# Kernel tuning notes

Hardware: AMD Instinct MI355X
Metric: run time of the kernel (lower is better)

The kernel has to match this reference:

```python
import jax, jax.numpy as jnp
import numpy as np

B, C_IN, C_OUT = 8, 64, 64
H, W = 256, 256
FH, FW = 16, 16  # patch grid from weight map spatial dims
HYPER_PARAMS = C_OUT * C_IN  # kernel_size=1, groups=1


def setup_inputs() -> dict:
    key = jax.random.key(0)
    kx, ks = jax.random.split(key)
    x = jax.random.normal(kx, (B, C_IN, H, W), dtype=jnp.float32)
    # s is the hypernetwork-generated per-patch weight map [b, out*in, fh, fw]
    s = jax.random.normal(ks, (B, HYPER_PARAMS, FH, FW), dtype=jnp.float32)
    return {"x": x, "s": s}


def reference(x, s):
    b, c, h, w = x.shape
    fh, fw = s.shape[-2], s.shape[-1]
    ph, pw = h // fh, w // fw
    out_ch = s.shape[1] // c  # hyper_params = out_ch * c (1x1 kernel, groups=1)
    # weight.permute(0,2,3,1).reshape(b*fh*fw*out, in, 1, 1) -> per-patch [out, in]
    Wp = jnp.transpose(s, (0, 2, 3, 1)).reshape(b, fh, fw, out_ch, c)
    # x.view(b,c,fh,ph,fw,pw).permute(0,2,4,1,3,5) -> per-patch blocks [b,fh,fw,c,ph,pw]
    xp = jnp.transpose(x.reshape(b, c, fh, ph, fw, pw), (0, 2, 4, 1, 3, 5))
    # grouped 1x1 conv over b*fh*fw groups == batched small matmul per patch
    y = jnp.einsum('bijoc,bijcpq->bijopq', Wp, xp)
    # .view(b,fh,fw,-1,ph,pw).permute(0,3,1,4,2,5).reshape(b,-1,h,w)
    return jnp.transpose(y, (0, 3, 1, 4, 2, 5)).reshape(b, out_ch, h, w)
```

## Files before the change

kernel.cpp:

```cpp
#include <hip/hip_runtime.h>

#define NB 8

typedef __bf16 bf16x8 __attribute__((ext_vector_type(8)));
typedef float  f32x4  __attribute__((ext_vector_type(4)));

__global__ __launch_bounds__(256) void fused_kernel(
    const float* __restrict__ x,
    const float* __restrict__ s,
    float* __restrict__ out)
{
    __shared__ char smem[49152];

    const int bid = blockIdx.x;
    const int b   = bid & 7;
    const int pjp = (bid >> 3) & 7;
    const int pi  = bid >> 6;
    const int t   = threadIdx.x;
    const int lane = t & 63;
    const int wv   = t >> 6;
    const int q    = lane & 15;
    const int hi   = lane >> 4;
    const int pat  = wv & 1;
    const int pgrp = wv >> 1;
    const int w0   = pjp * 32;
    const int pj0  = pjp * 2;

    const int sp_p = t >> 6;
    const int swq  = (t >> 3) & 7;
    const int sco  = t & 7;
    const float* xbase = x + (size_t)b * 4194304 + (size_t)(sco * 8) * 65536
                           + w0 + swq * 4;

    {
        const float2* sp2 = (const float2*)(s + (size_t)b * 1048576 + pi * 16 + pj0);
        #pragma unroll
        for (int k = 0; k < 16; ++k) {
            const int r = t + k * 256;
            float2 v = sp2[(size_t)r * 128];
            const int o = r >> 6, c = r & 63;
            const int ent = ((o >> 4) * 2 + (c >> 5)) * 64 + ((c >> 3) & 3) * 16 + (o & 15);
            const int byt = ent * 16 + (c & 7) * 2;
            *(__bf16*)(smem + byt)        = (__bf16)v.x;
            *(__bf16*)(smem + 8192 + byt) = (__bf16)v.y;
        }
    }

    {
        const int row0 = pi * 16;
        f32x4 v[8];
        #pragma unroll
        for (int cc = 0; cc < 8; ++cc)
            v[cc] = *(const f32x4*)(xbase + (size_t)cc * 65536
                                    + (size_t)(row0 + sp_p) * 256);
        #pragma unroll
        for (int i = 0; i < 4; ++i) {
            const int w = swq * 4 + i;
            bf16x8 e;
            #pragma unroll
            for (int cc = 0; cc < 8; ++cc) e[cc] = (__bf16)v[cc][i];
            *(bf16x8*)(smem + 16384 + sp_p * 4096 + w * 128
                       + ((sco * 16) ^ ((w & 7) << 4) ^ (sp_p << 4))) = e;
        }
    }
    __syncthreads();

    bf16x8 a[4][2];
    #pragma unroll
    for (int mt = 0; mt < 4; ++mt)
        #pragma unroll
        for (int kk = 0; kk < 2; ++kk)
            a[mt][kk] = *(const bf16x8*)(smem + pat * 8192
                          + ((mt * 2 + kk) * 64 + lane) * 16);

    int cur = 0;
    #pragma unroll
    for (int tile = 0; tile < 4; ++tile) {
        const int row0 = pi * 16 + tile * 4;
        char* bufc = smem + 16384 + cur * 16384;

        f32x4 nv[8];
        if (tile < 3) {
            #pragma unroll
            for (int cc = 0; cc < 8; ++cc)
                nv[cc] = *(const f32x4*)(xbase + (size_t)cc * 65536
                                         + (size_t)(row0 + 4 + sp_p) * 256);
        }
        __builtin_amdgcn_sched_barrier(0);

        bf16x8 bf[2][2];
        #pragma unroll
        for (int pp = 0; pp < 2; ++pp) {
            const int p = pgrp * 2 + pp;
            const int w = pat * 16 + q;
            #pragma unroll
            for (int kk = 0; kk < 2; ++kk) {
                const int co = kk * 4 + hi;
                bf[pp][kk] = *(const bf16x8*)(bufc + p * 4096 + w * 128
                              + ((co * 16) ^ ((w & 7) << 4) ^ (p << 4)));
            }
        }

        f32x4 acc[2][4];
        #pragma unroll
        for (int pp = 0; pp < 2; ++pp)
            #pragma unroll
            for (int mt = 0; mt < 4; ++mt) {
                acc[pp][mt] = (f32x4){0.f, 0.f, 0.f, 0.f};
                acc[pp][mt] = __builtin_amdgcn_mfma_f32_16x16x32_bf16(
                    a[mt][0], bf[pp][0], acc[pp][mt], 0, 0, 0);
                acc[pp][mt] = __builtin_amdgcn_mfma_f32_16x16x32_bf16(
                    a[mt][1], bf[pp][1], acc[pp][mt], 0, 0, 0);
            }

        if (tile < 3) {
            char* bufn = smem + 16384 + (cur ^ 1) * 16384;
            #pragma unroll
            for (int i = 0; i < 4; ++i) {
                const int w = swq * 4 + i;
                bf16x8 e;
                #pragma unroll
                for (int cc = 0; cc < 8; ++cc) e[cc] = (__bf16)nv[cc][i];
                *(bf16x8*)(bufn + sp_p * 4096 + w * 128
                           + ((sco * 16) ^ ((w & 7) << 4) ^ (sp_p << 4))) = e;
            }
        }
        __syncthreads();

        float* ef = (float*)bufc;
        #pragma unroll
        for (int h2 = 0; h2 < 2; ++h2) {
            #pragma unroll
            for (int pp = 0; pp < 2; ++pp) {
                const int p = pgrp * 2 + pp;
                const int w = pat * 16 + q;
                #pragma unroll
                for (int m2 = 0; m2 < 2; ++m2) {
                    const int mt = h2 * 2 + m2;
                    #pragma unroll
                    for (int r = 0; r < 4; ++r) {
                        const int o2 = m2 * 16 + hi * 4 + r;
                        ef[(o2 * 4 + p) * 32 + (w ^ ((o2 & 7) << 2))] = acc[pp][mt][r];
                    }
                }
            }
            __syncthreads();
            #pragma unroll
            for (int ps = 0; ps < 4; ++ps) {
                const int line = ps * 32 + (t >> 3);
                const int o2 = line >> 2, p = line & 3;
                f32x4 vv = *(const f32x4*)&ef[(o2 * 4 + p) * 32
                                              + ((sco * 4) ^ ((o2 & 7) << 2))];
                *(f32x4*)(out + (size_t)(b * 64 + h2 * 32 + o2) * 65536
                              + (size_t)(row0 + p) * 256 + w0 + sco * 4) = vv;
            }
            __syncthreads();
        }
        cur ^= 1;
    }
}

extern "C" void kernel_launch(void* const* d_in, const int* in_sizes, int n_in,
                              void* d_out, int out_size, void* d_ws, size_t ws_size,
                              hipStream_t stream)
{
    (void)in_sizes; (void)n_in; (void)out_size; (void)d_ws; (void)ws_size;
    const float* x = (const float*)d_in[0];
    const float* s = (const float*)d_in[1];
    float* out = (float*)d_out;

    fused_kernel<<<dim3(1024), dim3(256), 0, stream>>>(x, s, out);
}
```

Baseline: 77.59 us.

## Split each patch pair across two blocks and load all x rows upfront

Each block now handles 8 rows of a patch pair instead of 16, which doubles the grid to 2048 blocks. All global loads for x and s are issued at the start, before any conversion. The double-buffered 4-tile pipeline is replaced by a single tile with more MFMA work per wave. The goal is more memory parallelism and occupancy (launch bounds of 2) to hide latency, at the cost of loading the s weights twice per patch and holding more registers.

```diff
diff --git a/kernel.cpp b/kernel.cpp
--- a/kernel.cpp
+++ b/kernel.cpp
@@ -5,62 +5,70 @@
 typedef __bf16 bf16x8 __attribute__((ext_vector_type(8)));
 typedef float  f32x4  __attribute__((ext_vector_type(4)));
 
-__global__ __launch_bounds__(256) void fused_kernel(
+__global__ __launch_bounds__(256, 2) void fused_gemm(
     const float* __restrict__ x,
     const float* __restrict__ s,
     float* __restrict__ out)
 {
     __shared__ char smem[49152];
+    char* smemX = smem + 16384;
+    float* ef   = (float*)(smem + 16384);
 
     const int bid = blockIdx.x;
     const int b   = bid & 7;
-    const int pjp = (bid >> 3) & 7;
-    const int pi  = bid >> 6;
+    const int pi  = (bid >> 3) & 15;
+    const int ph  = (bid >> 7) & 1;
+    const int pjp = (bid >> 8) & 7;
     const int t   = threadIdx.x;
     const int lane = t & 63;
     const int wv   = t >> 6;
+    const int pat  = wv & 1;
+    const int wrow = wv >> 1;
     const int q    = lane & 15;
     const int hi   = lane >> 4;
-    const int pat  = wv & 1;
-    const int pgrp = wv >> 1;
     const int w0   = pjp * 32;
-    const int pj0  = pjp * 2;
+    const int row0 = pi * 16 + ph * 8;
 
-    const int sp_p = t >> 6;
-    const int swq  = (t >> 3) & 7;
-    const int sco  = t & 7;
-    const float* xbase = x + (size_t)b * 4194304 + (size_t)(sco * 8) * 65536
-                           + w0 + swq * 4;
+    const int swq = lane & 7;
+    const int sco = lane >> 3;
+    const float* xrowbase = x + (size_t)(b * 64 + sco * 8) * 65536
+                              + (size_t)row0 * 256 + w0 + swq * 4;
+    f32x4 xv[16];
+    #pragma unroll
+    for (int pp = 0; pp < 2; ++pp)
+        #pragma unroll
+        for (int cc = 0; cc < 8; ++cc)
+            xv[pp * 8 + cc] = *(const f32x4*)(xrowbase + (size_t)cc * 65536
+                                              + (size_t)(wv * 2 + pp) * 256);
 
-    {
-        const float2* sp2 = (const float2*)(s + (size_t)b * 1048576 + pi * 16 + pj0);
-        #pragma unroll
-        for (int k = 0; k < 16; ++k) {
-            const int r = t + k * 256;
-            float2 v = sp2[(size_t)r * 128];
-            const int o = r >> 6, c = r & 63;
-            const int ent = ((o >> 4) * 2 + (c >> 5)) * 64 + ((c >> 3) & 3) * 16 + (o & 15);
-            const int byt = ent * 16 + (c & 7) * 2;
-            *(__bf16*)(smem + byt)        = (__bf16)v.x;
-            *(__bf16*)(smem + 8192 + byt) = (__bf16)v.y;
-        }
+    const float2* sp2 = (const float2*)(s + (size_t)b * 1048576 + pi * 16 + pjp * 2);
+    float2 sv[16];
+    #pragma unroll
+    for (int k = 0; k < 16; ++k)
+        sv[k] = sp2[(size_t)(t + k * 256) * 128];
+
+    #pragma unroll
+    for (int k = 0; k < 16; ++k) {
+        const int r = t + k * 256;
+        const int o = r >> 6, c = r & 63;
+        const int ent = ((o >> 4) * 2 + (c >> 5)) * 64 + ((c >> 3) & 3) * 16 + (o & 15);
+        const int byt = ent * 16 + (c & 7) * 2;
+        *(__bf16*)(smem + byt)        = (__bf16)sv[k].x;
+        *(__bf16*)(smem + 8192 + byt) = (__bf16)sv[k].y;
     }
 
-    {
-        const int row0 = pi * 16;
-        f32x4 v[8];
-        #pragma unroll
-        for (int cc = 0; cc < 8; ++cc)
-            v[cc] = *(const f32x4*)(xbase + (size_t)cc * 65536
-                                    + (size_t)(row0 + sp_p) * 256);
+    #pragma unroll
+    for (int pp = 0; pp < 2; ++pp) {
+        const int p = wv * 2 + pp;
         #pragma unroll
         for (int i = 0; i < 4; ++i) {
             const int w = swq * 4 + i;
             bf16x8 e;
             #pragma unroll
-            for (int cc = 0; cc < 8; ++cc) e[cc] = (__bf16)v[cc][i];
-            *(bf16x8*)(smem + 16384 + sp_p * 4096 + w * 128
-                       + ((sco * 16) ^ ((w & 7) << 4) ^ (sp_p << 4))) = e;
+            for (int cc = 0; cc < 8; ++cc)
+                e[cc] = (__bf16)xv[pp * 8 + cc][i];
+            *(bf16x8*)(smemX + p * 4096 + w * 128
+                       + ((sco * 16) ^ ((w & 7) << 4) ^ ((p & 7) << 4))) = e;
         }
     }
     __syncthreads();
@@ -73,90 +81,68 @@
             a[mt][kk] = *(const bf16x8*)(smem + pat * 8192
                           + ((mt * 2 + kk) * 64 + lane) * 16);
 
-    int cur = 0;
+    bf16x8 bfrag[4][2];
     #pragma unroll
-    for (int tile = 0; tile < 4; ++tile) {
-        const int row0 = pi * 16 + tile * 4;
-        char* bufc = smem + 16384 + cur * 16384;
+    for (int nt = 0; nt < 4; ++nt) {
+        const int p = wrow * 4 + nt;
+        const int w = pat * 16 + q;
+        #pragma unroll
+        for (int kk = 0; kk < 2; ++kk) {
+            const int co = kk * 4 + hi;
+            bfrag[nt][kk] = *(const bf16x8*)(smemX + p * 4096 + w * 128
+                            + ((co * 16) ^ ((w & 7) << 4) ^ ((p & 7) << 4)));
+        }
+    }
+    __syncthreads();
 
-        f32x4 nv[8];
-        if (tile < 3) {
+    const int u2t = t >> 3;
+    const int wq2 = t & 7;
+    #pragma unroll
+    for (int h2 = 0; h2 < 2; ++h2) {
+        f32x4 acc[2][4];
+        #pragma unroll
+        for (int m2 = 0; m2 < 2; ++m2)
             #pragma unroll
-            for (int cc = 0; cc < 8; ++cc)
-                nv[cc] = *(const f32x4*)(xbase + (size_t)cc * 65536
-                                         + (size_t)(row0 + 4 + sp_p) * 256);
-        }
-        __builtin_amdgcn_sched_barrier(0);
+            for (int nt = 0; nt < 4; ++nt)
+                acc[m2][nt] = (f32x4){0.f, 0.f, 0.f, 0.f};
 
-        bf16x8 bf[2][2];
         #pragma unroll
-        for (int pp = 0; pp < 2; ++pp) {
-            const int p = pgrp * 2 + pp;
-            const int w = pat * 16 + q;
+        for (int m2 = 0; m2 < 2; ++m2) {
+            const int mt = h2 * 2 + m2;
             #pragma unroll
-            for (int kk = 0; kk < 2; ++kk) {
-                const int co = kk * 4 + hi;
-                bf[pp][kk] = *(const bf16x8*)(bufc + p * 4096 + w * 128
-                              + ((co * 16) ^ ((w & 7) << 4) ^ (p << 4)));
+            for (int nt = 0; nt < 4; ++nt) {
+                acc[m2][nt] = __builtin_amdgcn_mfma_f32_16x16x32_bf16(
+                    a[mt][0], bfrag[nt][0], acc[m2][nt], 0, 0, 0);
+                acc[m2][nt] = __builtin_amdgcn_mfma_f32_16x16x32_bf16(
+                    a[mt][1], bfrag[nt][1], acc[m2][nt], 0, 0, 0);
             }
         }
 
-        f32x4 acc[2][4];
         #pragma unroll
-        for (int pp = 0; pp < 2; ++pp)
+        for (int m2 = 0; m2 < 2; ++m2)
             #pragma unroll
-            for (int mt = 0; mt < 4; ++mt) {
-                acc[pp][mt] = (f32x4){0.f, 0.f, 0.f, 0.f};
-                acc[pp][mt] = __builtin_amdgcn_mfma_f32_16x16x32_bf16(
-                    a[mt][0], bf[pp][0], acc[pp][mt], 0, 0, 0);
-                acc[pp][mt] = __builtin_amdgcn_mfma_f32_16x16x32_bf16(
-                    a[mt][1], bf[pp][1], acc[pp][mt], 0, 0, 0);
+            for (int nt = 0; nt < 4; ++nt) {
+                const int p = wrow * 4 + nt;
+                #pragma unroll
+                for (int r = 0; r < 4; ++r) {
+                    const int o2 = m2 * 16 + hi * 4 + r;
+                    const int w  = pat * 16 + q;
+                    ef[(o2 * 8 + p) * 32 + (w ^ ((o2 & 7) << 2))] = acc[m2][nt][r];
+                }
             }
-
-        if (tile < 3) {
-            char* bufn = smem + 16384 + (cur ^ 1) * 16384;
-            #pragma unroll
-            for (int i = 0; i < 4; ++i) {
-                const int w = swq * 4 + i;
-                bf16x8 e;
-                #pragma unroll
-                for (int cc = 0; cc < 8; ++cc) e[cc] = (__bf16)nv[cc][i];
-                *(bf16x8*)(bufn + sp_p * 4096 + w * 128
-                           + ((sco * 16) ^ ((w & 7) << 4) ^ (sp_p << 4))) = e;
-            }
-        }
         __syncthreads();
 
-        float* ef = (float*)bufc;
         #pragma unroll
-        for (int h2 = 0; h2 < 2; ++h2) {
-            #pragma unroll
-            for (int pp = 0; pp < 2; ++pp) {
-                const int p = pgrp * 2 + pp;
-                const int w = pat * 16 + q;
-                #pragma unroll
-                for (int m2 = 0; m2 < 2; ++m2) {
-                    const int mt = h2 * 2 + m2;
-                    #pragma unroll
-                    for (int r = 0; r < 4; ++r) {
-                        const int o2 = m2 * 16 + hi * 4 + r;
-                        ef[(o2 * 4 + p) * 32 + (w ^ ((o2 & 7) << 2))] = acc[pp][mt][r];
-                    }
-                }
-            }
-            __syncthreads();
-            #pragma unroll
-            for (int ps = 0; ps < 4; ++ps) {
-                const int line = ps * 32 + (t >> 3);
-                const int o2 = line >> 2, p = line & 3;
-                f32x4 vv = *(const f32x4*)&ef[(o2 * 4 + p) * 32
-                                              + ((sco * 4) ^ ((o2 & 7) << 2))];
-                *(f32x4*)(out + (size_t)(b * 64 + h2 * 32 + o2) * 65536
-                              + (size_t)(row0 + p) * 256 + w0 + sco * 4) = vv;
-            }
-            __syncthreads();
+        for (int ps = 0; ps < 8; ++ps) {
+            const int r2 = ps * 32 + u2t;
+            const int o2 = r2 >> 3;
+            const int p  = r2 & 7;
+            f32x4 vv = *(const f32x4*)&ef[(o2 * 8 + p) * 32
+                                          + ((wq2 * 4) ^ ((o2 & 7) << 2))];
+            *(f32x4*)(out + (size_t)(b * 64 + h2 * 32 + o2) * 65536
+                          + (size_t)(row0 + p) * 256 + w0 + wq2 * 4) = vv;
         }
-        cur ^= 1;
+        if (h2 == 0) __syncthreads();
     }
 }
 
@@ -169,5 +155,5 @@
     const float* s = (const float*)d_in[1];
     float* out = (float*)d_out;
 
-    fused_kernel<<<dim3(1024), dim3(256), 0, stream>>>(x, s, out);
+    fused_gemm<<<dim3(2048), dim3(256), 0, stream>>>(x, s, out);
 }
```

Result: slower. 92.31 us (+19.0%).
